# Kernel tuning notes

Measured on AMD Instinct MI355X. Metric: run time of the kernel, lower is better.

The kernel has to match this reference:

```python
import jax, jax.numpy as jnp
import numpy as np


def setup_inputs() -> dict:
    key = jax.random.key(0)
    ks = jax.random.split(key, 8)
    B, N, M = 8, 4096, 4096
    return {
        "R": jax.random.normal(ks[0], (B, 3, 3), dtype=jnp.float32),
        "t": jax.random.normal(ks[1], (B, 3), dtype=jnp.float32),
        "S": jax.random.uniform(ks[2], (B,), dtype=jnp.float32),
        "R_g": jax.random.normal(ks[3], (B, 3, 3), dtype=jnp.float32),
        "t_g": jax.random.normal(ks[4], (B, 3), dtype=jnp.float32),
        "S_g": jax.random.uniform(ks[5], (B,), dtype=jnp.float32),
        "T_X": jax.random.normal(ks[6], (B, N, 3), dtype=jnp.float32),
        "Y": jax.random.normal(ks[7], (B, M, 3), dtype=jnp.float32),
    }


def _chamfer(x, y):
    # x: [B,N,3], y: [B,M,3]. Pairwise Euclidean distances [B,N,M] via the
    x2 = jnp.sum(x * x, axis=-1)                      # [B,N]
    y2 = jnp.sum(y * y, axis=-1)                      # [B,M]
    xy = jnp.einsum('bnd,bmd->bnm', x, y)             # [B,N,M]
    d2 = x2[:, :, None] + y2[:, None, :] - 2.0 * xy
    dist = jnp.sqrt(jnp.maximum(d2, 0.0))             # [B,N,M]
    min_x_to_y = jnp.min(dist, axis=2)                # [B,N]
    min_y_to_x = jnp.min(dist, axis=1)                # [B,M]
    per_batch = jnp.mean(min_x_to_y, axis=1) + jnp.mean(min_y_to_x, axis=1)
    return jnp.mean(per_batch)


def _registration(R, t, S, R_g, t_g, S_g):
    eye = jnp.eye(3, dtype=R.dtype)
    diff = jnp.einsum('bji,bjk->bik', R_g, R) - eye   # R_g^T @ R - I, [B,3,3]
    L_R = jnp.sum(diff * diff, axis=(1, 2))           # squared Frobenius norm
    L_t = jnp.sum((t_g - t) ** 2, axis=1)
    L_S = (S_g - S) ** 2
    return jnp.mean(L_R + L_t + L_S)


def reference(R, t, S, R_g, t_g, S_g, T_X, Y):
    L_R = _registration(R, t, S, R_g, t_g, S_g)
    L_CD = _chamfer(T_X, Y)
    return (L_R + L_CD, L_R, L_CD)
```

## Files before the change

### kernel.cpp

```cpp
#include <hip/hip_runtime.h>
#include <hip/hip_bf16.h>

constexpr int B_ = 8;
constexpr int N_ = 4096;
constexpr int M_ = 4096;
constexpr int TPB = 256;
constexpr int QPT = 4;
constexpr int QPB = TPB * QPT;
constexpr int QBLKS = N_ / QPB;
constexpr int SPLIT = 16;
constexpr int CHUNK = M_ / SPLIT;
constexpr int NPAIR = CHUNK / 2;
constexpr int NQ = 2 * B_ * N_;

typedef float v2f __attribute__((ext_vector_type(2)));

static __device__ __forceinline__ v2f pk_fma(v2f a, v2f b, v2f c) {
    v2f d;
    asm("v_pk_fma_f32 %0, %1, %2, %3" : "=v"(d) : "v"(a), "v"(b), "v"(c));
    return d;
}

__global__ __launch_bounds__(TPB) void chamfer_pass1(
    const float* __restrict__ X, const float* __restrict__ Yp,
    float* __restrict__ part)
{
    __shared__ float sdb8[NPAIR * 8];

    int bid = blockIdx.x;
    const int dir   = bid & 1;             bid >>= 1;
    const int chunk = bid & (SPLIT - 1);   bid >>= 4;
    const int qblk  = bid & (QBLKS - 1);   bid >>= 2;
    const int b     = bid;

    const float* q  = dir ? Yp : X;
    const float* db = dir ? X  : Yp;

    const int t = threadIdx.x;

    {
        const float* src = db + (size_t)(b * M_ + chunk * CHUNK + t) * 3;
        float a0 = src[0], a1 = src[1], a2 = src[2];
        const int base = (t >> 1) * 8 + (t & 1);
        sdb8[base + 0] = -2.0f * a0;
        sdb8[base + 2] = -2.0f * a1;
        sdb8[base + 4] = -2.0f * a2;
        sdb8[base + 6] = a0 * a0 + a1 * a1 + a2 * a2;
    }

    v2f qxx[QPT], qyy[QPT], qzz[QPT];
    float qn[QPT];
    const int qbase = b * N_ + qblk * QPB;
    #pragma unroll
    for (int k = 0; k < QPT; ++k) {
        const float* qp = q + (size_t)(qbase + k * TPB + t) * 3;
        float x = qp[0], y = qp[1], z = qp[2];
        qxx[k] = (v2f){x, x};
        qyy[k] = (v2f){y, y};
        qzz[k] = (v2f){z, z};
        qn[k]  = x * x + y * y + z * z;
    }
    __syncthreads();

    const v2f* s2 = (const v2f*)sdb8;
    const float BIG = 3.0e38f;
    float mA[QPT], mB[QPT], mC[QPT], mD[QPT];
    #pragma unroll
    for (int k = 0; k < QPT; ++k) { mA[k] = BIG; mB[k] = BIG; mC[k] = BIG; mD[k] = BIG; }

    #pragma unroll 2
    for (int j = 0; j < NPAIR; j += 2) {
        v2f xx0 = s2[4 * j + 0], yy0 = s2[4 * j + 1];
        v2f zz0 = s2[4 * j + 2], ww0 = s2[4 * j + 3];
        v2f xx1 = s2[4 * j + 4], yy1 = s2[4 * j + 5];
        v2f zz1 = s2[4 * j + 6], ww1 = s2[4 * j + 7];
        #pragma unroll
        for (int k = 0; k < QPT; ++k) {
            v2f d0 = pk_fma(qxx[k], xx0, pk_fma(qyy[k], yy0, pk_fma(qzz[k], zz0, ww0)));
            v2f d1 = pk_fma(qxx[k], xx1, pk_fma(qyy[k], yy1, pk_fma(qzz[k], zz1, ww1)));
            mA[k] = fminf(mA[k], d0.x);
            mB[k] = fminf(mB[k], d0.y);
            mC[k] = fminf(mC[k], d1.x);
            mD[k] = fminf(mD[k], d1.y);
        }
    }

    const int wbase = chunk * NQ + dir * (B_ * N_) + qbase;
    #pragma unroll
    for (int k = 0; k < QPT; ++k) {
        float m = fminf(fminf(mA[k], mB[k]), fminf(mC[k], mD[k]));
        part[wbase + k * TPB + t] = fmaxf(m + qn[k], 0.0f);
    }
}

__global__ __launch_bounds__(TPB) void finalize_fused(
    const float* __restrict__ part,
    const float* __restrict__ R,  const float* __restrict__ t,
    const float* __restrict__ S,  const float* __restrict__ Rg,
    const float* __restrict__ tg, const float* __restrict__ Sg,
    float* __restrict__ out)
{
    __shared__ float wsum[TPB / 64];
    __shared__ float sreg[8];
    const int tid = threadIdx.x;
    const int qid = blockIdx.x * TPB + tid;

    float m = part[qid];
    #pragma unroll
    for (int c = 1; c < SPLIT; ++c) m = fminf(m, part[c * NQ + qid]);
    float d = sqrtf(m);

    #pragma unroll
    for (int off = 32; off > 0; off >>= 1) d += __shfl_down(d, off, 64);
    if ((tid & 63) == 0) wsum[tid >> 6] = d;

    if (blockIdx.x == 0 && tid < 8) {
        const float* Rb  = R  + tid * 9;
        const float* Rgb = Rg + tid * 9;
        float acc = 0.0f;
        #pragma unroll
        for (int i = 0; i < 3; ++i) {
            #pragma unroll
            for (int k = 0; k < 3; ++k) {
                float v = 0.0f;
                #pragma unroll
                for (int j = 0; j < 3; ++j)
                    v = fmaf(Rgb[j * 3 + i], Rb[j * 3 + k], v);
                if (i == k) v -= 1.0f;
                acc = fmaf(v, v, acc);
            }
        }
        #pragma unroll
        for (int dd = 0; dd < 3; ++dd) {
            float dv = tg[tid * 3 + dd] - t[tid * 3 + dd];
            acc = fmaf(dv, dv, acc);
        }
        float dS = Sg[tid] - S[tid];
        acc = fmaf(dS, dS, acc);
        sreg[tid] = acc;
    }
    __syncthreads();

    if (tid == 0) {
        float bs = (wsum[0] + wsum[1] + wsum[2] + wsum[3]) * (1.0f / (B_ * N_));
        atomicAdd(&out[0], bs);
        atomicAdd(&out[2], bs);
        if (blockIdx.x == 0) {
            float rs = 0.0f;
            #pragma unroll
            for (int bb = 0; bb < 8; ++bb) rs += sreg[bb];
            float L_R = rs * (1.0f / B_);
            atomicAdd(&out[0], L_R);
            atomicAdd(&out[1], L_R);
        }
    }
}

extern "C" void kernel_launch(void* const* d_in, const int* in_sizes, int n_in,
                              void* d_out, int out_size, void* d_ws, size_t ws_size,
                              hipStream_t stream) {
    const float* R  = (const float*)d_in[0];
    const float* t  = (const float*)d_in[1];
    const float* S  = (const float*)d_in[2];
    const float* Rg = (const float*)d_in[3];
    const float* tg = (const float*)d_in[4];
    const float* Sg = (const float*)d_in[5];
    const float* X  = (const float*)d_in[6];
    const float* Yp = (const float*)d_in[7];
    float* out = (float*)d_out;

    float* part = (float*)d_ws;

    hipMemsetAsync(out, 0, 3 * sizeof(float), stream);
    chamfer_pass1<<<2 * B_ * QBLKS * SPLIT, TPB, 0, stream>>>(X, Yp, part);
    finalize_fused<<<NQ / TPB, TPB, 0, stream>>>(part, R, t, S, Rg, tg, Sg, out);
}
```

Baseline: 95.78 us.

## Compute chamfer distances with fp16 MFMA and fold output zeroing into kernel

Rewrites the pairwise-distance pass to use the 16x16x32 f16 MFMA instruction. Each query is encoded as [x,y,z,1] and each database point as [-2x,-2y,-2z,|p|^2] in fp16, zero-padded, and only lanes 0-15 supply real data. The database split drops from 16 chunks to 2 halves, so finalize reads two partials instead of sixteen, and the memset launch is replaced by zeroing inside the first block. This trades the packed-FP32 FMA loop for matrix-core throughput, at the cost of fp16 precision on coordinates and norms, which may shift the result beyond tolerance. Zeroing the output inside the kernel relies on block 0 running before any finalize atomics, which holds because finalize is a separate later launch.

```diff
diff --git a/kernel.cpp b/kernel.cpp
--- a/kernel.cpp
+++ b/kernel.cpp
@@ -5,92 +5,132 @@
 constexpr int N_ = 4096;
 constexpr int M_ = 4096;
 constexpr int TPB = 256;
-constexpr int QPT = 4;
-constexpr int QPB = TPB * QPT;
-constexpr int QBLKS = N_ / QPB;
-constexpr int SPLIT = 16;
-constexpr int CHUNK = M_ / SPLIT;
-constexpr int NPAIR = CHUNK / 2;
+constexpr int HALF_PTS = 2048;
+constexpr int NTILE = HALF_PTS / 16;
 constexpr int NQ = 2 * B_ * N_;
 
-typedef float v2f __attribute__((ext_vector_type(2)));
-
-static __device__ __forceinline__ v2f pk_fma(v2f a, v2f b, v2f c) {
-    v2f d;
-    asm("v_pk_fma_f32 %0, %1, %2, %3" : "=v"(d) : "v"(a), "v"(b), "v"(c));
-    return d;
-}
-
-__global__ __launch_bounds__(TPB) void chamfer_pass1(
+typedef _Float16 half8 __attribute__((ext_vector_type(8)));
+typedef float    f32x4 __attribute__((ext_vector_type(4)));
+
+__global__ __launch_bounds__(TPB) void chamfer_mfma(
     const float* __restrict__ X, const float* __restrict__ Yp,
-    float* __restrict__ part)
+    float* __restrict__ part, float* __restrict__ out)
 {
-    __shared__ float sdb8[NPAIR * 8];
+    __shared__ half8 sB[HALF_PTS + 1];
+
+    if (blockIdx.x == 0 && threadIdx.x < 3) out[threadIdx.x] = 0.0f;
 
     int bid = blockIdx.x;
-    const int dir   = bid & 1;             bid >>= 1;
-    const int chunk = bid & (SPLIT - 1);   bid >>= 4;
-    const int qblk  = bid & (QBLKS - 1);   bid >>= 2;
-    const int b     = bid;
+    const int dir    = bid & 1;   bid >>= 1;
+    const int half_  = bid & 1;   bid >>= 1;
+    const int qchunk = bid & 15;  bid >>= 4;
+    const int b      = bid;
 
     const float* q  = dir ? Yp : X;
     const float* db = dir ? X  : Yp;
 
-    const int t = threadIdx.x;
-
-    {
-        const float* src = db + (size_t)(b * M_ + chunk * CHUNK + t) * 3;
-        float a0 = src[0], a1 = src[1], a2 = src[2];
-        const int base = (t >> 1) * 8 + (t & 1);
-        sdb8[base + 0] = -2.0f * a0;
-        sdb8[base + 2] = -2.0f * a1;
-        sdb8[base + 4] = -2.0f * a2;
-        sdb8[base + 6] = a0 * a0 + a1 * a1 + a2 * a2;
-    }
-
-    v2f qxx[QPT], qyy[QPT], qzz[QPT];
-    float qn[QPT];
-    const int qbase = b * N_ + qblk * QPB;
-    #pragma unroll
-    for (int k = 0; k < QPT; ++k) {
-        const float* qp = q + (size_t)(qbase + k * TPB + t) * 3;
-        float x = qp[0], y = qp[1], z = qp[2];
-        qxx[k] = (v2f){x, x};
-        qyy[k] = (v2f){y, y};
-        qzz[k] = (v2f){z, z};
-        qn[k]  = x * x + y * y + z * z;
+    const int tid  = threadIdx.x;
+    const int lane = tid & 63;
+    const int wave = tid >> 6;
+    const int l15  = lane & 15;
+
+    const int dbbase = b * M_ + half_ * HALF_PTS;
+    #pragma unroll
+    for (int k = 0; k < 8; ++k) {
+        const int pt = tid + k * TPB;
+        const float* pp = db + (size_t)(dbbase + pt) * 3;
+        float px = pp[0], py = pp[1], pz = pp[2];
+        float pn = px * px + py * py + pz * pz;
+        half8 v;
+        v[0] = (_Float16)(-2.0f * px);
+        v[1] = (_Float16)(-2.0f * py);
+        v[2] = (_Float16)(-2.0f * pz);
+        v[3] = (_Float16)pn;
+        v[4] = (_Float16)0.0f; v[5] = (_Float16)0.0f;
+        v[6] = (_Float16)0.0f; v[7] = (_Float16)0.0f;
+        sB[pt] = v;
+    }
+    if (tid == 0) {
+        half8 z;
+        #pragma unroll
+        for (int i = 0; i < 8; ++i) z[i] = (_Float16)0.0f;
+        sB[HALF_PTS] = z;
+    }
+
+    const int qglob = b * N_ + qchunk * 256 + wave * 64;
+    half8 af[4];
+    #pragma unroll
+    for (int f = 0; f < 4; ++f) {
+        half8 v;
+        #pragma unroll
+        for (int i = 0; i < 8; ++i) v[i] = (_Float16)0.0f;
+        if (lane < 16) {
+            const float* qp = q + (size_t)(qglob + f * 16 + l15) * 3;
+            v[0] = (_Float16)qp[0];
+            v[1] = (_Float16)qp[1];
+            v[2] = (_Float16)qp[2];
+            v[3] = (_Float16)1.0f;
+        }
+        af[f] = v;
     }
     __syncthreads();
 
-    const v2f* s2 = (const v2f*)sdb8;
+    const half8* bp = sB + ((lane < 16) ? l15 : HALF_PTS);
+    const int step  = (lane < 16) ? 16 : 0;
+
+    f32x4 zero4; zero4[0] = 0.f; zero4[1] = 0.f; zero4[2] = 0.f; zero4[3] = 0.f;
     const float BIG = 3.0e38f;
-    float mA[QPT], mB[QPT], mC[QPT], mD[QPT];
-    #pragma unroll
-    for (int k = 0; k < QPT; ++k) { mA[k] = BIG; mB[k] = BIG; mC[k] = BIG; mD[k] = BIG; }
-
-    #pragma unroll 2
-    for (int j = 0; j < NPAIR; j += 2) {
-        v2f xx0 = s2[4 * j + 0], yy0 = s2[4 * j + 1];
-        v2f zz0 = s2[4 * j + 2], ww0 = s2[4 * j + 3];
-        v2f xx1 = s2[4 * j + 4], yy1 = s2[4 * j + 5];
-        v2f zz1 = s2[4 * j + 6], ww1 = s2[4 * j + 7];
-        #pragma unroll
-        for (int k = 0; k < QPT; ++k) {
-            v2f d0 = pk_fma(qxx[k], xx0, pk_fma(qyy[k], yy0, pk_fma(qzz[k], zz0, ww0)));
-            v2f d1 = pk_fma(qxx[k], xx1, pk_fma(qyy[k], yy1, pk_fma(qzz[k], zz1, ww1)));
-            mA[k] = fminf(mA[k], d0.x);
-            mB[k] = fminf(mB[k], d0.y);
-            mC[k] = fminf(mC[k], d1.x);
-            mD[k] = fminf(mD[k], d1.y);
-        }
-    }
-
-    const int wbase = chunk * NQ + dir * (B_ * N_) + qbase;
-    #pragma unroll
-    for (int k = 0; k < QPT; ++k) {
-        float m = fminf(fminf(mA[k], mB[k]), fminf(mC[k], mD[k]));
-        part[wbase + k * TPB + t] = fmaxf(m + qn[k], 0.0f);
-    }
+    float rm[4][4];
+    #pragma unroll
+    for (int f = 0; f < 4; ++f)
+        #pragma unroll
+        for (int i = 0; i < 4; ++i) rm[f][i] = BIG;
+
+    for (int t = 0; t < NTILE; t += 2) {
+        half8 b0 = bp[0];
+        half8 b1 = bp[step];
+        bp += (step << 1);
+        f32x4 a0[4], a1[4];
+        #pragma unroll
+        for (int f = 0; f < 4; ++f)
+            a0[f] = __builtin_amdgcn_mfma_f32_16x16x32_f16(af[f], b0, zero4, 0, 0, 0);
+        #pragma unroll
+        for (int f = 0; f < 4; ++f)
+            a1[f] = __builtin_amdgcn_mfma_f32_16x16x32_f16(af[f], b1, zero4, 0, 0, 0);
+        #pragma unroll
+        for (int f = 0; f < 4; ++f)
+            #pragma unroll
+            for (int i = 0; i < 4; ++i)
+                rm[f][i] = fminf(rm[f][i], fminf(a0[f][i], a1[f][i]));
+    }
+
+    #pragma unroll
+    for (int f = 0; f < 4; ++f)
+        #pragma unroll
+        for (int i = 0; i < 4; ++i) {
+            float v = rm[f][i];
+            v = fminf(v, __shfl_xor(v, 1, 64));
+            v = fminf(v, __shfl_xor(v, 2, 64));
+            v = fminf(v, __shfl_xor(v, 4, 64));
+            v = fminf(v, __shfl_xor(v, 8, 64));
+            rm[f][i] = v;
+        }
+
+    const int f_sel = (lane >> 2) & 3;
+    const int i_sel = lane & 3;
+    float v = BIG;
+    #pragma unroll
+    for (int f = 0; f < 4; ++f)
+        #pragma unroll
+        for (int i = 0; i < 4; ++i)
+            if (f == f_sel && i == i_sel) v = rm[f][i];
+
+    const int j  = f_sel * 16 + ((lane >> 4) << 2) + i_sel;
+    const int qs = qchunk * 256 + wave * 64 + j;
+    const float* qp = q + (size_t)(b * N_ + qs) * 3;
+    const float qn = qp[0] * qp[0] + qp[1] * qp[1] + qp[2] * qp[2];
+    const float d2 = fmaxf(v + qn, 0.0f);
+    part[half_ * NQ + dir * (B_ * N_) + b * N_ + qs] = d2;
 }
 
 __global__ __launch_bounds__(TPB) void finalize_fused(
@@ -105,9 +145,7 @@
     const int tid = threadIdx.x;
     const int qid = blockIdx.x * TPB + tid;
 
-    float m = part[qid];
-    #pragma unroll
-    for (int c = 1; c < SPLIT; ++c) m = fminf(m, part[c * NQ + qid]);
+    float m = fminf(part[qid], part[NQ + qid]);
     float d = sqrtf(m);
 
     #pragma unroll
@@ -124,8 +162,8 @@
             for (int k = 0; k < 3; ++k) {
                 float v = 0.0f;
                 #pragma unroll
-                for (int j = 0; j < 3; ++j)
-                    v = fmaf(Rgb[j * 3 + i], Rb[j * 3 + k], v);
+                for (int jj = 0; jj < 3; ++jj)
+                    v = fmaf(Rgb[jj * 3 + i], Rb[jj * 3 + k], v);
                 if (i == k) v -= 1.0f;
                 acc = fmaf(v, v, acc);
             }
@@ -171,7 +209,6 @@
 
     float* part = (float*)d_ws;
 
-    hipMemsetAsync(out, 0, 3 * sizeof(float), stream);
-    chamfer_pass1<<<2 * B_ * QBLKS * SPLIT, TPB, 0, stream>>>(X, Yp, part);
+    chamfer_mfma<<<2 * 2 * 16 * B_, TPB, 0, stream>>>(X, Yp, part, out);
     finalize_fused<<<NQ / TPB, TPB, 0, stream>>>(part, R, t, S, Rg, tg, Sg, out);
 }
```

Result: faster. 93.53 us (-2.4%).
